# Performance work log

Measured on AMD Instinct MI355X. Metric: run time of the kernel, lower is better.

The kernel has to match this reference:

```python
import jax, jax.numpy as jnp
import numpy as np
from jax import lax

N = 4096
B = 4


def setup_inputs() -> dict:
    key = jax.random.key(0)
    k1, k2 = jax.random.split(key)
    preds = jax.random.uniform(k1, (B, N), dtype=jnp.float32)  # seed infection probs in [0,1)
    adj = jax.random.uniform(k2, (N, N), dtype=jnp.float32)    # edge infection probs in [0,1)
    return {"preds": preds, "adj": adj, "niter": 3}


def reference(preds, adj, niter):
    # Original per-sample loop vectorized over batch:
    #   P2 = adj.T * pred[None, :]            -> adj.T[i, j] * pred[j] = adj[j, i] * pred[j]
    #   pred_new[i] = 1 - prod_j (1 - P2[i, j])  (independent-cascade update)
    At = adj.T  # [N, N]

    def step(p, _):
        # p: [B, N]; broadcast to [B, N, N], product-reduce over source nodes j (last axis)
        p_new = 1.0 - jnp.prod(1.0 - At[None, :, :] * p[:, None, :], axis=2)
        return p_new, None

    out, _ = lax.scan(step, preds, None, length=niter)
    return out  # [B, N]
```

## Files before the change

### kernel.cpp

```cpp
#include <hip/hip_runtime.h>


#define N 4096
#define B 4
#define CHUNKS 256
#define JC (N / CHUNKS)
#define T1 256
#define ITILE (T1 * 4)
#define IPANELS (N / ITILE)

__global__ __launch_bounds__(T1, 4) void diffusion_stage1(
    const float* __restrict__ adj,
    const float* __restrict__ p,
    float* __restrict__ partial) {
    __shared__ __align__(16) float lds_p[JC][B];

    const int tid = threadIdx.x;
    const int i0  = blockIdx.x * ITILE + tid * 4;
    const int j0  = blockIdx.y * JC;

    if (tid < JC * B) {
        int j = tid >> 2, b = tid & 3;
        lds_p[j][b] = p[b * N + j0 + j];
    }
    __syncthreads();

    float4 acc[B];
#pragma unroll
    for (int b = 0; b < B; ++b) acc[b] = make_float4(1.f, 1.f, 1.f, 1.f);

    const float* aptr = adj + (size_t)j0 * N + i0;

    float4 buf[JC];
#pragma unroll
    for (int k = 0; k < JC; ++k)
        buf[k] = *reinterpret_cast<const float4*>(aptr + (size_t)k * N);
    __builtin_amdgcn_sched_barrier(0);

#pragma unroll
    for (int j = 0; j < JC; ++j) {
        float4 a  = buf[j];
        float4 pv = *reinterpret_cast<const float4*>(&lds_p[j][0]);
        const float pb[4] = {pv.x, pv.y, pv.z, pv.w};
#pragma unroll
        for (int b = 0; b < B; ++b) {
            acc[b].x *= fmaf(-a.x, pb[b], 1.f);
            acc[b].y *= fmaf(-a.y, pb[b], 1.f);
            acc[b].z *= fmaf(-a.z, pb[b], 1.f);
            acc[b].w *= fmaf(-a.w, pb[b], 1.f);
        }
    }

    const int c = blockIdx.y;
#pragma unroll
    for (int b = 0; b < B; ++b) {
        *reinterpret_cast<float4*>(partial + ((size_t)(c * B + b)) * N + i0) = acc[b];
    }
}

__global__ __launch_bounds__(T1) void diffusion_stage2(
    const float* __restrict__ partial,
    float* __restrict__ pout) {
    int t = blockIdx.x * T1 + threadIdx.x;
    int b = t >> 12;
    int i = t & (N - 1);
    float prod = 1.f;
#pragma unroll 16
    for (int c = 0; c < CHUNKS; ++c)
        prod *= partial[((size_t)(c * B + b)) * N + i];
    pout[t] = 1.f - prod;
}

__global__ __launch_bounds__(256) void diffusion_full(
    const float* __restrict__ adj, const float* __restrict__ p,
    float* __restrict__ pout) {
    int i = blockIdx.x * 256 + threadIdx.x;
    float acc[B] = {1.f, 1.f, 1.f, 1.f};
    for (int j = 0; j < N; ++j) {
        float a = adj[(size_t)j * N + i];
#pragma unroll
        for (int b = 0; b < B; ++b) acc[b] *= fmaf(-a, p[b * N + j], 1.f);
    }
#pragma unroll
    for (int b = 0; b < B; ++b) pout[b * N + i] = 1.f - acc[b];
}

extern "C" void kernel_launch(void* const* d_in, const int* in_sizes, int n_in,
                              void* d_out, int out_size, void* d_ws, size_t ws_size,
                              hipStream_t stream) {
    const float* preds = (const float*)d_in[0];
    const float* adj   = (const float*)d_in[1];
    float* out = (float*)d_out;

    float* p0      = (float*)d_ws;
    float* partial = p0 + (size_t)B * N;

    const size_t need = ((size_t)B * N + (size_t)CHUNKS * B * N) * sizeof(float);

    if (ws_size >= need) {
        dim3 g1(IPANELS, CHUNKS), b1(T1);
        dim3 g2((B * N) / T1), b2(T1);
        diffusion_stage1<<<g1, b1, 0, stream>>>(adj, preds, partial);
        diffusion_stage2<<<g2, b2, 0, stream>>>(partial, out);
        diffusion_stage1<<<g1, b1, 0, stream>>>(adj, out, partial);
        diffusion_stage2<<<g2, b2, 0, stream>>>(partial, p0);
        diffusion_stage1<<<g1, b1, 0, stream>>>(adj, p0, partial);
        diffusion_stage2<<<g2, b2, 0, stream>>>(partial, out);
    } else {
        dim3 g(N / 256), b(256);
        diffusion_full<<<g, b, 0, stream>>>(adj, preds, out);
        diffusion_full<<<g, b, 0, stream>>>(adj, out, p0);
        diffusion_full<<<g, b, 0, stream>>>(adj, p0, out);
    }
}
```

Measured before the change: 156.2 us.

## Convert adjacency to bf16 once and store partial products in bf16

Adds a pre-pass that converts the fp32 adjacency matrix to bf16 in workspace. The three diffusion iterations then stream half the bytes, and the per-chunk partial products are also written and read as bf16. The aim is to cut the memory traffic of the bandwidth-bound stage1/stage2 kernels. The trade-off is an extra full read of the 64MB matrix plus a 32MB write, and a loss of precision in both the adjacency values and the partial products, which can hurt accuracy after the 256-way product.

```diff
diff --git a/kernel.cpp b/kernel.cpp
--- a/kernel.cpp
+++ b/kernel.cpp
@@ -6,17 +6,40 @@
 #define CHUNKS 256
 #define JC (N / CHUNKS)
 #define T1 256
-#define ITILE (T1 * 4)
+#define TN 4
+#define ITILE (T1 * TN)
 #define IPANELS (N / ITILE)
 
+typedef unsigned int   uint_t;
+typedef unsigned short ushort_t;
+
+__device__ __forceinline__ ushort_t f2bf(float f) {
+    uint_t u = __float_as_uint(f);
+    return (ushort_t)((u + 0x7FFFu + ((u >> 16) & 1u)) >> 16);
+}
+__device__ __forceinline__ float bf_lo(uint_t w) { return __uint_as_float(w << 16); }
+__device__ __forceinline__ float bf_hi(uint_t w) { return __uint_as_float(w & 0xFFFF0000u); }
+
+__global__ __launch_bounds__(256) void conv_bf16(
+    const float4* __restrict__ src, uint4* __restrict__ dst) {
+    size_t t = (size_t)blockIdx.x * 256 + threadIdx.x;
+    float4 a = src[2 * t], b = src[2 * t + 1];
+    uint4 o;
+    o.x = (uint_t)f2bf(a.x) | ((uint_t)f2bf(a.y) << 16);
+    o.y = (uint_t)f2bf(a.z) | ((uint_t)f2bf(a.w) << 16);
+    o.z = (uint_t)f2bf(b.x) | ((uint_t)f2bf(b.y) << 16);
+    o.w = (uint_t)f2bf(b.z) | ((uint_t)f2bf(b.w) << 16);
+    dst[t] = o;
+}
+
 __global__ __launch_bounds__(T1, 4) void diffusion_stage1(
-    const float* __restrict__ adj,
+    const uint2* __restrict__ adjb,
     const float* __restrict__ p,
-    float* __restrict__ partial) {
+    uint2* __restrict__ partial) {
     __shared__ __align__(16) float lds_p[JC][B];
 
     const int tid = threadIdx.x;
-    const int i0  = blockIdx.x * ITILE + tid * 4;
+    const int i0  = blockIdx.x * ITILE + tid * TN;
     const int j0  = blockIdx.y * JC;
 
     if (tid < JC * B) {
@@ -29,37 +52,41 @@
 #pragma unroll
     for (int b = 0; b < B; ++b) acc[b] = make_float4(1.f, 1.f, 1.f, 1.f);
 
-    const float* aptr = adj + (size_t)j0 * N + i0;
+    const uint2* aptr = adjb + ((size_t)j0 * N + i0) / 4;
 
-    float4 buf[JC];
+    uint2 buf[JC];
 #pragma unroll
     for (int k = 0; k < JC; ++k)
-        buf[k] = *reinterpret_cast<const float4*>(aptr + (size_t)k * N);
+        buf[k] = aptr[(size_t)k * (N / 4)];
     __builtin_amdgcn_sched_barrier(0);
 
 #pragma unroll
     for (int j = 0; j < JC; ++j) {
-        float4 a  = buf[j];
+        const float e0 = bf_lo(buf[j].x), e1 = bf_hi(buf[j].x);
+        const float e2 = bf_lo(buf[j].y), e3 = bf_hi(buf[j].y);
         float4 pv = *reinterpret_cast<const float4*>(&lds_p[j][0]);
         const float pb[4] = {pv.x, pv.y, pv.z, pv.w};
 #pragma unroll
         for (int b = 0; b < B; ++b) {
-            acc[b].x *= fmaf(-a.x, pb[b], 1.f);
-            acc[b].y *= fmaf(-a.y, pb[b], 1.f);
-            acc[b].z *= fmaf(-a.z, pb[b], 1.f);
-            acc[b].w *= fmaf(-a.w, pb[b], 1.f);
+            acc[b].x *= fmaf(-e0, pb[b], 1.f);
+            acc[b].y *= fmaf(-e1, pb[b], 1.f);
+            acc[b].z *= fmaf(-e2, pb[b], 1.f);
+            acc[b].w *= fmaf(-e3, pb[b], 1.f);
         }
     }
 
     const int c = blockIdx.y;
 #pragma unroll
     for (int b = 0; b < B; ++b) {
-        *reinterpret_cast<float4*>(partial + ((size_t)(c * B + b)) * N + i0) = acc[b];
+        uint2 pp;
+        pp.x = (uint_t)f2bf(acc[b].x) | ((uint_t)f2bf(acc[b].y) << 16);
+        pp.y = (uint_t)f2bf(acc[b].z) | ((uint_t)f2bf(acc[b].w) << 16);
+        partial[(((size_t)(c * B + b)) * N + i0) / 4] = pp;
     }
 }
 
 __global__ __launch_bounds__(T1) void diffusion_stage2(
-    const float* __restrict__ partial,
+    const ushort_t* __restrict__ partial,
     float* __restrict__ pout) {
     int t = blockIdx.x * T1 + threadIdx.x;
     int b = t >> 12;
@@ -67,7 +94,7 @@
     float prod = 1.f;
 #pragma unroll 16
     for (int c = 0; c < CHUNKS; ++c)
-        prod *= partial[((size_t)(c * B + b)) * N + i];
+        prod *= __uint_as_float((uint_t)partial[((size_t)(c * B + b)) * N + i] << 16);
     pout[t] = 1.f - prod;
 }
 
@@ -92,24 +119,30 @@
     const float* adj   = (const float*)d_in[1];
     float* out = (float*)d_out;
 
-    float* p0      = (float*)d_ws;
-    float* partial = p0 + (size_t)B * N;
+    uint_t* adjb      = (uint_t*)d_ws;
+    ushort_t* partial = (ushort_t*)((char*)d_ws + (size_t)N * N * 2);
+    float* p0         = (float*)((char*)partial + (size_t)CHUNKS * B * N * 2);
 
-    const size_t need = ((size_t)B * N + (size_t)CHUNKS * B * N) * sizeof(float);
+    const size_t need = (size_t)N * N * 2 + (size_t)CHUNKS * B * N * 2
+                      + (size_t)B * N * sizeof(float);
 
     if (ws_size >= need) {
+        conv_bf16<<<(unsigned)((size_t)N * N / 8 / 256), 256, 0, stream>>>(
+            (const float4*)adj, (uint4*)adjb);
+
         dim3 g1(IPANELS, CHUNKS), b1(T1);
         dim3 g2((B * N) / T1), b2(T1);
-        diffusion_stage1<<<g1, b1, 0, stream>>>(adj, preds, partial);
+        diffusion_stage1<<<g1, b1, 0, stream>>>((const uint2*)adjb, preds, (uint2*)partial);
         diffusion_stage2<<<g2, b2, 0, stream>>>(partial, out);
-        diffusion_stage1<<<g1, b1, 0, stream>>>(adj, out, partial);
+        diffusion_stage1<<<g1, b1, 0, stream>>>((const uint2*)adjb, out, (uint2*)partial);
         diffusion_stage2<<<g2, b2, 0, stream>>>(partial, p0);
-        diffusion_stage1<<<g1, b1, 0, stream>>>(adj, p0, partial);
+        diffusion_stage1<<<g1, b1, 0, stream>>>((const uint2*)adjb, p0, (uint2*)partial);
         diffusion_stage2<<<g2, b2, 0, stream>>>(partial, out);
     } else {
+        float* q0 = (float*)d_ws;
         dim3 g(N / 256), b(256);
         diffusion_full<<<g, b, 0, stream>>>(adj, preds, out);
-        diffusion_full<<<g, b, 0, stream>>>(adj, out, p0);
-        diffusion_full<<<g, b, 0, stream>>>(adj, p0, out);
+        diffusion_full<<<g, b, 0, stream>>>(adj, out, q0);
+        diffusion_full<<<g, b, 0, stream>>>(adj, q0, out);
     }
 }
```

Result: faster. 149.0 us (-4.6%).
